# Optimization experiments

Measured on AMD Instinct MI355X. Metric: run time of the kernel, lower is better.

Reference implementation:

```python
import jax, jax.numpy as jnp
import numpy as np

N = 2048   # atoms (m == n from einsum structure)
F = 64     # dist_exp_size
H = 128    # atom_emb_size
K = 256    # hidden_size


def setup_inputs() -> dict:
    key = jax.random.key(0)
    k1, k2, k3, k4, k5 = jax.random.split(key, 5)
    dist_adj = jax.random.uniform(k1, (N, N), dtype=jnp.float32)
    dist_exp = jax.random.normal(k2, (N, N, F), dtype=jnp.float32)
    atom_emb = jax.random.normal(k3, (N, H), dtype=jnp.float32)
    # parameters: torch.rand -> uniform [0,1)
    bilinear_w = jax.random.uniform(k4, (F, H, K), dtype=jnp.float32)
    bilinear_b = jax.random.uniform(k5, (K,), dtype=jnp.float32)
    return {"dist_adj": dist_adj, "dist_exp": dist_exp, "atom_emb": atom_emb,
            "bilinear_w": bilinear_w, "bilinear_b": bilinear_b}


def reference(dist_adj, dist_exp, atom_emb, bilinear_w, bilinear_b):
    # adjacency-weighted aggregation over neighbors: [n, f]
    adj_exp = jnp.einsum('mn,mnf->mf', dist_adj, dist_exp)
    # trilinear bilinear contraction per node: [n, k]
    feat = jnp.einsum('nf,fhk,nh->nk', adj_exp, bilinear_w, atom_emb)
    # softplus activation, then bias added AFTER activation (faithful to source)
    return jax.nn.softplus(feat) + bilinear_b
```

## Files before the change

kernel.cpp:

```cpp
#include <hip/hip_runtime.h>
#include <hip/hip_bf16.h>

#define N_ATOMS 2048
#define F_DIM   64
#define H_DIM   128
#define K_DIM   256
#define KD      8192
#define BM 32
#define BN 64
#define BK 128
#define NT (KD / BK)

typedef __attribute__((ext_vector_type(8))) short short8;
typedef __attribute__((ext_vector_type(4))) float f32x4;
typedef __attribute__((ext_vector_type(8))) unsigned short ushort8v;

static __device__ __forceinline__ unsigned short f2bf(float x) {
  unsigned int u = __float_as_uint(x);
  u += 0x7fff + ((u >> 16) & 1);
  return (unsigned short)(u >> 16);
}

__global__ __launch_bounds__(256) void adj_exp_kernel(
    const float* __restrict__ dist_adj,
    const float* __restrict__ dist_exp,
    float* __restrict__ adj_exp) {
  const int m  = blockIdx.x;
  const int t  = threadIdx.x;
  const int f4 = t & 15;
  const int ng = t >> 4;

  const float* __restrict__ arow = dist_adj + (size_t)m * N_ATOMS;
  const float* __restrict__ base = dist_exp + (size_t)m * N_ATOMS * F_DIM + f4 * 4;

  float4 acc = make_float4(0.f, 0.f, 0.f, 0.f);
  #pragma unroll 4
  for (int n = ng; n < N_ATOMS; n += 16) {
    float a  = arow[n];
    float4 v = *(const float4*)(base + (size_t)n * F_DIM);
    acc.x += a * v.x; acc.y += a * v.y; acc.z += a * v.z; acc.w += a * v.w;
  }

  __shared__ float4 red[16][16];
  red[ng][f4] = acc;
  __syncthreads();
  if (t < 16) {
    float4 s = red[0][t];
    #pragma unroll
    for (int g = 1; g < 16; ++g) {
      float4 v = red[g][t];
      s.x += v.x; s.y += v.y; s.z += v.z; s.w += v.w;
    }
    *(float4*)(adj_exp + m * F_DIM + t * 4) = s;
  }
}

__global__ __launch_bounds__(256) void wt_kernel(
    const float* __restrict__ W,
    unsigned short* __restrict__ Wt) {
  const int kb = blockIdx.x;
  const int cb = blockIdx.y;
  const int t  = threadIdx.x;

  __shared__ float tile[128][68];

  {
    const int r0 = t >> 4;
    const int c4 = (t & 15) * 4;
    #pragma unroll
    for (int i = 0; i < 8; ++i) {
      const int r = i * 16 + r0;
      float4 v = *(const float4*)(W + (size_t)(kb * 128 + r) * K_DIM + cb * 64 + c4);
      tile[r][c4 + 0] = v.x; tile[r][c4 + 1] = v.y;
      tile[r][c4 + 2] = v.z; tile[r][c4 + 3] = v.w;
    }
  }
  __syncthreads();
  {
    char* outb = (char*)Wt + (size_t)((cb << 6) | kb) * 16384;
    #pragma unroll
    for (int j = 0; j < 4; ++j) {
      const int o   = t * 64 + j * 16;
      const int cc  = o >> 8;
      const int r0b = (o & 255) ^ ((cc & 7) << 4);
      const int kk0 = r0b >> 1;
      ushort8v v;
      #pragma unroll
      for (int e = 0; e < 8; ++e) v[e] = f2bf(tile[kk0 + e][cc]);
      *(ushort8v*)(outb + o) = v;
    }
  }
}

__global__ __launch_bounds__(256) void bilinear_kernel(
    const float* __restrict__ adj_exp,
    const float* __restrict__ emb,
    const unsigned short* __restrict__ Wt,
    const float* __restrict__ bias,
    float* __restrict__ out) {
  const int b  = blockIdx.x;
  const int wg = (b & 7) * 32 + (b >> 3);
  const int mb = wg & 63;
  const int cb = wg >> 6;
  const int m0 = mb * BM;
  const int c0 = cb * BN;

  const int t  = threadIdx.x;
  const int w  = t >> 6;
  const int l  = t & 63;
  const int lr = l & 15;
  const int lg = l >> 4;

  __shared__ __align__(16) unsigned short Bl[2][8192];
  __shared__ __align__(16) unsigned short Al[2][BM][136];
  __shared__ float adjT[F_DIM][BM];

  const char* wt_base = (const char*)Wt;
  #define STAGE_B(buf, step)                                                      \
    {                                                                             \
      const char* src = wt_base + (size_t)((cb << 6) | (step)) * 16384;           \
      char* dstb = (char*)&Bl[(buf)][0];                                          \
      _Pragma("unroll")                                                           \
      for (int i = 0; i < 4; ++i) {                                               \
        const int chunk = i * 4 + w;                                              \
        __builtin_amdgcn_global_load_lds(                                         \
            (const __attribute__((address_space(1))) unsigned int*)(src + chunk * 1024 + l * 16), \
            (__attribute__((address_space(3))) unsigned int*)(dstb + chunk * 1024), \
            16, 0, 0);                                                            \
      }                                                                           \
    }

  const int arow = t >> 3;
  const int hc   = (t & 7) * 16;
  #define STAGE_A(buf, step)                                                      \
    {                                                                             \
      const float s = adjT[(step)][arow];                                         \
      ushort8v lo, hi;                                                            \
      _Pragma("unroll")                                                           \
      for (int i = 0; i < 8; ++i) {                                               \
        lo[i] = f2bf(s * er[i]);                                                  \
        hi[i] = f2bf(s * er[8 + i]);                                              \
      }                                                                           \
      *(ushort8v*)&Al[(buf)][arow][hc]     = lo;                                  \
      *(ushort8v*)&Al[(buf)][arow][hc + 8] = hi;                                  \
    }

  STAGE_B(0, 0);

  float er[16];
  {
    const float* ep = emb + (size_t)(m0 + arow) * H_DIM + hc;
    #pragma unroll
    for (int i = 0; i < 4; ++i) {
      float4 e = *(const float4*)(ep + i * 4);
      er[i * 4 + 0] = e.x; er[i * 4 + 1] = e.y;
      er[i * 4 + 2] = e.z; er[i * 4 + 3] = e.w;
    }
  }
  {
    const int r  = t & 31;
    const int f0 = (t >> 5) * 8;
    float4 a0 = *(const float4*)(adj_exp + (size_t)(m0 + r) * F_DIM + f0);
    float4 a1 = *(const float4*)(adj_exp + (size_t)(m0 + r) * F_DIM + f0 + 4);
    adjT[f0 + 0][r] = a0.x; adjT[f0 + 1][r] = a0.y;
    adjT[f0 + 2][r] = a0.z; adjT[f0 + 3][r] = a0.w;
    adjT[f0 + 4][r] = a1.x; adjT[f0 + 5][r] = a1.y;
    adjT[f0 + 6][r] = a1.z; adjT[f0 + 7][r] = a1.w;
  }
  __syncthreads();

  STAGE_A(0, 0);
  __syncthreads();

  f32x4 acc0 = {0.f, 0.f, 0.f, 0.f};
  f32x4 acc1 = {0.f, 0.f, 0.f, 0.f};
  const int ccol = w * 16 + lr;
  const int bswz = (lr & 7) << 4;

  int cur = 0;
  #pragma unroll 1
  for (int ts = 0; ts < NT; ++ts) {
    const int nxt = cur ^ 1;
    if (ts + 1 < NT) {
      STAGE_B(nxt, ts + 1);
      STAGE_A(nxt, ts + 1);
      asm volatile("s_waitcnt vmcnt(4)" ::: "memory");
    } else {
      asm volatile("s_waitcnt vmcnt(0)" ::: "memory");
    }
    asm volatile("s_waitcnt lgkmcnt(0)" ::: "memory");
    __builtin_amdgcn_s_barrier();
    asm volatile("" ::: "memory");

    const char* Bbase = (const char*)&Bl[cur][0];
    #pragma unroll
    for (int ks = 0; ks < 4; ++ks) {
      const int boff = ccol * 256 + ((ks * 64 + lg * 16) ^ bswz);
      short8 bf = *(const short8*)(Bbase + boff);
      short8 a0 = *(const short8*)&Al[cur][lr][ks * 32 + lg * 8];
      short8 a1 = *(const short8*)&Al[cur][16 + lr][ks * 32 + lg * 8];
      acc0 = __builtin_amdgcn_mfma_f32_16x16x32_bf16(a0, bf, acc0, 0, 0, 0);
      acc1 = __builtin_amdgcn_mfma_f32_16x16x32_bf16(a1, bf, acc1, 0, 0, 0);
    }

    asm volatile("s_waitcnt lgkmcnt(0)" ::: "memory");
    __builtin_amdgcn_s_barrier();
    asm volatile("" ::: "memory");
    cur = nxt;
  }
  #undef STAGE_A
  #undef STAGE_B

  const int col = c0 + ccol;
  const float bb = bias[col];
  #pragma unroll
  for (int r = 0; r < 4; ++r) {
    const int row0 = m0 + lg * 4 + r;
    float x0  = acc0[r];
    float sp0 = (x0 > 20.f) ? x0 : ((x0 < -20.f) ? __expf(x0) : log1pf(__expf(x0)));
    out[(size_t)row0 * K_DIM + col] = sp0 + bb;
    const int row1 = row0 + 16;
    float x1  = acc1[r];
    float sp1 = (x1 > 20.f) ? x1 : ((x1 < -20.f) ? __expf(x1) : log1pf(__expf(x1)));
    out[(size_t)row1 * K_DIM + col] = sp1 + bb;
  }
}

extern "C" void kernel_launch(void* const* d_in, const int* in_sizes, int n_in,
                              void* d_out, int out_size, void* d_ws, size_t ws_size,
                              hipStream_t stream) {
  const float* dist_adj   = (const float*)d_in[0];
  const float* dist_exp   = (const float*)d_in[1];
  const float* atom_emb   = (const float*)d_in[2];
  const float* bilinear_w = (const float*)d_in[3];
  const float* bilinear_b = (const float*)d_in[4];
  float* out = (float*)d_out;

  float* adj_exp = (float*)d_ws;
  unsigned short* Wt =
      (unsigned short*)((char*)d_ws + (size_t)N_ATOMS * F_DIM * sizeof(float));

  hipLaunchKernelGGL(adj_exp_kernel, dim3(N_ATOMS), dim3(256), 0, stream,
                     dist_adj, dist_exp, adj_exp);
  hipLaunchKernelGGL(wt_kernel, dim3(NT, K_DIM / BN), dim3(256), 0, stream,
                     bilinear_w, Wt);
  hipLaunchKernelGGL(bilinear_kernel, dim3((N_ATOMS / BM) * (K_DIM / BN)), dim3(256), 0, stream,
                     adj_exp, atom_emb, Wt, bilinear_b, out);
}
```

Measured before the change: 237.7 us.

## Fuse prep kernels and factor adj scaling out of bilinear MFMA

The adjacency-aggregation and weight-transpose kernels are merged into one launch, with the weight part split into half-tiles. The aggregation now stages the adjacency row in shared memory and uses nontemporal loads for the streamed dist_exp. In the bilinear kernel, atom embeddings are converted to bf16 once and kept in registers as MFMA A operands. The per-f adjacency scale is applied to the fp32 MFMA partial result instead of building scaled A tiles in LDS every step, which removes per-step conversion work, LDS writes and one barrier wait. It adds per-step partial accumulators and slightly changes rounding, since the scale is no longer applied before the bf16 conversion.

```diff
diff --git a/kernel.cpp b/kernel.cpp
--- a/kernel.cpp
+++ b/kernel.cpp
@@ -21,73 +21,83 @@
   return (unsigned short)(u >> 16);
 }
 
-__global__ __launch_bounds__(256) void adj_exp_kernel(
+__global__ __launch_bounds__(256) void fused_prep_kernel(
     const float* __restrict__ dist_adj,
     const float* __restrict__ dist_exp,
-    float* __restrict__ adj_exp) {
-  const int m  = blockIdx.x;
-  const int t  = threadIdx.x;
-  const int f4 = t & 15;
-  const int ng = t >> 4;
-
-  const float* __restrict__ arow = dist_adj + (size_t)m * N_ATOMS;
-  const float* __restrict__ base = dist_exp + (size_t)m * N_ATOMS * F_DIM + f4 * 4;
-
-  float4 acc = make_float4(0.f, 0.f, 0.f, 0.f);
-  #pragma unroll 4
-  for (int n = ng; n < N_ATOMS; n += 16) {
-    float a  = arow[n];
-    float4 v = *(const float4*)(base + (size_t)n * F_DIM);
-    acc.x += a * v.x; acc.y += a * v.y; acc.z += a * v.z; acc.w += a * v.w;
-  }
-
-  __shared__ float4 red[16][16];
-  red[ng][f4] = acc;
-  __syncthreads();
-  if (t < 16) {
-    float4 s = red[0][t];
-    #pragma unroll
-    for (int g = 1; g < 16; ++g) {
-      float4 v = red[g][t];
-      s.x += v.x; s.y += v.y; s.z += v.z; s.w += v.w;
-    }
-    *(float4*)(adj_exp + m * F_DIM + t * 4) = s;
-  }
-}
-
-__global__ __launch_bounds__(256) void wt_kernel(
     const float* __restrict__ W,
+    float* __restrict__ adj_exp,
     unsigned short* __restrict__ Wt) {
-  const int kb = blockIdx.x;
-  const int cb = blockIdx.y;
-  const int t  = threadIdx.x;
-
-  __shared__ float tile[128][68];
-
-  {
-    const int r0 = t >> 4;
-    const int c4 = (t & 15) * 4;
-    #pragma unroll
-    for (int i = 0; i < 8; ++i) {
-      const int r = i * 16 + r0;
-      float4 v = *(const float4*)(W + (size_t)(kb * 128 + r) * K_DIM + cb * 64 + c4);
-      tile[r][c4 + 0] = v.x; tile[r][c4 + 1] = v.y;
-      tile[r][c4 + 2] = v.z; tile[r][c4 + 3] = v.w;
-    }
-  }
-  __syncthreads();
-  {
-    char* outb = (char*)Wt + (size_t)((cb << 6) | kb) * 16384;
-    #pragma unroll
-    for (int j = 0; j < 4; ++j) {
-      const int o   = t * 64 + j * 16;
-      const int cc  = o >> 8;
-      const int r0b = (o & 255) ^ ((cc & 7) << 4);
-      const int kk0 = r0b >> 1;
-      ushort8v v;
-      #pragma unroll
-      for (int e = 0; e < 8; ++e) v[e] = f2bf(tile[kk0 + e][cc]);
-      *(ushort8v*)(outb + o) = v;
+  __shared__ __align__(16) char smem[17408];
+  const int t = threadIdx.x;
+
+  if (blockIdx.x < 512) {
+    const int q    = blockIdx.x;
+    const int cb   = q >> 7;
+    const int kb   = (q >> 1) & 63;
+    const int half = q & 1;
+    float (*tile)[68] = (float(*)[68])smem;
+
+    {
+      const int r0 = t >> 4;
+      const int c4 = (t & 15) * 4;
+      #pragma unroll
+      for (int i = 0; i < 4; ++i) {
+        const int r = i * 16 + r0;
+        f32x4 v = *(const f32x4*)(W + (size_t)(kb * 128 + half * 64 + r) * K_DIM + cb * 64 + c4);
+        tile[r][c4 + 0] = v[0]; tile[r][c4 + 1] = v[1];
+        tile[r][c4 + 2] = v[2]; tile[r][c4 + 3] = v[3];
+      }
+    }
+    __syncthreads();
+    {
+      char* outb = (char*)Wt + (size_t)((cb << 6) | kb) * 16384;
+      #pragma unroll
+      for (int j = 0; j < 2; ++j) {
+        const int lin  = t * 32 + j * 16;
+        const int cc   = lin >> 7;
+        const int w128 = lin & 127;
+        const int k0   = (w128 ^ ((cc & 7) << 4)) >> 1;
+        ushort8v v;
+        #pragma unroll
+        for (int e = 0; e < 8; ++e) v[e] = f2bf(tile[k0 + e][cc]);
+        *(ushort8v*)(outb + cc * 256 + half * 128 + w128) = v;
+      }
+    }
+  } else {
+    const int m  = blockIdx.x - 512;
+    const int f4 = t & 15;
+    const int ng = t >> 4;
+
+    float* arowl = (float*)smem;
+    f32x4* red   = (f32x4*)(smem + 8192);
+
+    {
+      const f32x4* src = (const f32x4*)(dist_adj + (size_t)m * N_ATOMS);
+      f32x4* dst = (f32x4*)arowl;
+      #pragma unroll
+      for (int i = 0; i < 2; ++i) {
+        const int idx = i * 256 + t;
+        dst[idx] = __builtin_nontemporal_load(src + idx);
+      }
+    }
+    __syncthreads();
+
+    const float* __restrict__ base = dist_exp + (size_t)m * N_ATOMS * F_DIM + f4 * 4;
+    f32x4 acc = {0.f, 0.f, 0.f, 0.f};
+    #pragma unroll 4
+    for (int n = ng; n < N_ATOMS; n += 16) {
+      float a  = arowl[n];
+      f32x4 v = __builtin_nontemporal_load((const f32x4*)(base + (size_t)n * F_DIM));
+      acc += a * v;
+    }
+
+    red[ng * 16 + f4] = acc;
+    __syncthreads();
+    if (t < 16) {
+      f32x4 s = red[t];
+      #pragma unroll
+      for (int g = 1; g < 16; ++g) s += red[g * 16 + t];
+      *(f32x4*)(adj_exp + m * F_DIM + t * 4) = s;
     }
   }
 }
@@ -112,8 +122,7 @@
   const int lg = l >> 4;
 
   __shared__ __align__(16) unsigned short Bl[2][8192];
-  __shared__ __align__(16) unsigned short Al[2][BM][136];
-  __shared__ float adjT[F_DIM][BM];
+  __shared__ __align__(16) float adjT[F_DIM][BM];
 
   const char* wt_base = (const char*)Wt;
   #define STAGE_B(buf, step)                                                      \
@@ -130,50 +139,37 @@
       }                                                                           \
     }
 
-  const int arow = t >> 3;
-  const int hc   = (t & 7) * 16;
-  #define STAGE_A(buf, step)                                                      \
-    {                                                                             \
-      const float s = adjT[(step)][arow];                                         \
-      ushort8v lo, hi;                                                            \
-      _Pragma("unroll")                                                           \
-      for (int i = 0; i < 8; ++i) {                                               \
-        lo[i] = f2bf(s * er[i]);                                                  \
-        hi[i] = f2bf(s * er[8 + i]);                                              \
-      }                                                                           \
-      *(ushort8v*)&Al[(buf)][arow][hc]     = lo;                                  \
-      *(ushort8v*)&Al[(buf)][arow][hc + 8] = hi;                                  \
-    }
-
   STAGE_B(0, 0);
 
-  float er[16];
-  {
-    const float* ep = emb + (size_t)(m0 + arow) * H_DIM + hc;
+  short8 Ef0[4], Ef1[4];
+  #pragma unroll
+  for (int ks = 0; ks < 4; ++ks) {
+    const float* p0 = emb + (size_t)(m0 + lr) * H_DIM + ks * 32 + lg * 8;
+    const float* p1 = emb + (size_t)(m0 + 16 + lr) * H_DIM + ks * 32 + lg * 8;
+    f32x4 u0 = *(const f32x4*)p0, u1 = *(const f32x4*)(p0 + 4);
+    f32x4 v0 = *(const f32x4*)p1, v1 = *(const f32x4*)(p1 + 4);
+    short8 e0, e1;
     #pragma unroll
     for (int i = 0; i < 4; ++i) {
-      float4 e = *(const float4*)(ep + i * 4);
-      er[i * 4 + 0] = e.x; er[i * 4 + 1] = e.y;
-      er[i * 4 + 2] = e.z; er[i * 4 + 3] = e.w;
-    }
+      e0[i]     = (short)f2bf(u0[i]); e0[4 + i] = (short)f2bf(u1[i]);
+      e1[i]     = (short)f2bf(v0[i]); e1[4 + i] = (short)f2bf(v1[i]);
+    }
+    Ef0[ks] = e0; Ef1[ks] = e1;
   }
   {
     const int r  = t & 31;
     const int f0 = (t >> 5) * 8;
-    float4 a0 = *(const float4*)(adj_exp + (size_t)(m0 + r) * F_DIM + f0);
-    float4 a1 = *(const float4*)(adj_exp + (size_t)(m0 + r) * F_DIM + f0 + 4);
-    adjT[f0 + 0][r] = a0.x; adjT[f0 + 1][r] = a0.y;
-    adjT[f0 + 2][r] = a0.z; adjT[f0 + 3][r] = a0.w;
-    adjT[f0 + 4][r] = a1.x; adjT[f0 + 5][r] = a1.y;
-    adjT[f0 + 6][r] = a1.z; adjT[f0 + 7][r] = a1.w;
+    f32x4 a0 = *(const f32x4*)(adj_exp + (size_t)(m0 + r) * F_DIM + f0);
+    f32x4 a1 = *(const f32x4*)(adj_exp + (size_t)(m0 + r) * F_DIM + f0 + 4);
+    adjT[f0 + 0][r] = a0[0]; adjT[f0 + 1][r] = a0[1];
+    adjT[f0 + 2][r] = a0[2]; adjT[f0 + 3][r] = a0[3];
+    adjT[f0 + 4][r] = a1[0]; adjT[f0 + 5][r] = a1[1];
+    adjT[f0 + 6][r] = a1[2]; adjT[f0 + 7][r] = a1[3];
   }
   __syncthreads();
 
-  STAGE_A(0, 0);
-  __syncthreads();
-
-  f32x4 acc0 = {0.f, 0.f, 0.f, 0.f};
-  f32x4 acc1 = {0.f, 0.f, 0.f, 0.f};
+  f32x4 facc0 = {0.f, 0.f, 0.f, 0.f};
+  f32x4 facc1 = {0.f, 0.f, 0.f, 0.f};
   const int ccol = w * 16 + lr;
   const int bswz = (lr & 7) << 4;
 
@@ -183,32 +179,34 @@
     const int nxt = cur ^ 1;
     if (ts + 1 < NT) {
       STAGE_B(nxt, ts + 1);
-      STAGE_A(nxt, ts + 1);
       asm volatile("s_waitcnt vmcnt(4)" ::: "memory");
     } else {
       asm volatile("s_waitcnt vmcnt(0)" ::: "memory");
     }
-    asm volatile("s_waitcnt lgkmcnt(0)" ::: "memory");
     __builtin_amdgcn_s_barrier();
     asm volatile("" ::: "memory");
 
+    f32x4 a0 = *(const f32x4*)&adjT[ts][lg * 4];
+    f32x4 a1 = *(const f32x4*)&adjT[ts][16 + lg * 4];
+
     const char* Bbase = (const char*)&Bl[cur][0];
+    f32x4 t0 = {0.f, 0.f, 0.f, 0.f};
+    f32x4 t1 = {0.f, 0.f, 0.f, 0.f};
     #pragma unroll
     for (int ks = 0; ks < 4; ++ks) {
       const int boff = ccol * 256 + ((ks * 64 + lg * 16) ^ bswz);
       short8 bf = *(const short8*)(Bbase + boff);
-      short8 a0 = *(const short8*)&Al[cur][lr][ks * 32 + lg * 8];
-      short8 a1 = *(const short8*)&Al[cur][16 + lr][ks * 32 + lg * 8];
-      acc0 = __builtin_amdgcn_mfma_f32_16x16x32_bf16(a0, bf, acc0, 0, 0, 0);
-      acc1 = __builtin_amdgcn_mfma_f32_16x16x32_bf16(a1, bf, acc1, 0, 0, 0);
-    }
+      t0 = __builtin_amdgcn_mfma_f32_16x16x32_bf16(Ef0[ks], bf, t0, 0, 0, 0);
+      t1 = __builtin_amdgcn_mfma_f32_16x16x32_bf16(Ef1[ks], bf, t1, 0, 0, 0);
+    }
+    facc0 += a0 * t0;
+    facc1 += a1 * t1;
 
     asm volatile("s_waitcnt lgkmcnt(0)" ::: "memory");
     __builtin_amdgcn_s_barrier();
     asm volatile("" ::: "memory");
     cur = nxt;
   }
-  #undef STAGE_A
   #undef STAGE_B
 
   const int col = c0 + ccol;
@@ -216,11 +214,11 @@
   #pragma unroll
   for (int r = 0; r < 4; ++r) {
     const int row0 = m0 + lg * 4 + r;
-    float x0  = acc0[r];
+    float x0  = facc0[r];
     float sp0 = (x0 > 20.f) ? x0 : ((x0 < -20.f) ? __expf(x0) : log1pf(__expf(x0)));
     out[(size_t)row0 * K_DIM + col] = sp0 + bb;
     const int row1 = row0 + 16;
-    float x1  = acc1[r];
+    float x1  = facc1[r];
     float sp1 = (x1 > 20.f) ? x1 : ((x1 < -20.f) ? __expf(x1) : log1pf(__expf(x1)));
     out[(size_t)row1 * K_DIM + col] = sp1 + bb;
   }
@@ -240,10 +238,8 @@
   unsigned short* Wt =
       (unsigned short*)((char*)d_ws + (size_t)N_ATOMS * F_DIM * sizeof(float));
 
-  hipLaunchKernelGGL(adj_exp_kernel, dim3(N_ATOMS), dim3(256), 0, stream,
-                     dist_adj, dist_exp, adj_exp);
-  hipLaunchKernelGGL(wt_kernel, dim3(NT, K_DIM / BN), dim3(256), 0, stream,
-                     bilinear_w, Wt);
+  hipLaunchKernelGGL(fused_prep_kernel, dim3(512 + N_ATOMS), dim3(256), 0, stream,
+                     dist_adj, dist_exp, bilinear_w, adj_exp, Wt);
   hipLaunchKernelGGL(bilinear_kernel, dim3((N_ATOMS / BM) * (K_DIM / BN)), dim3(256), 0, stream,
                      adj_exp, atom_emb, Wt, bilinear_b, out);
 }
```

New measurement: 225.5 us. -5.1%, faster.
